# Optimization experiments

Hardware: AMD Instinct MI355X
Metric: run time of the kernel (lower is better)

## Reference

```python
import jax, jax.numpy as jnp
import numpy as np

SEQ, B, I, H = 2048, 64, 512, 512


def setup_inputs() -> dict:
    key = jax.random.key(0)
    ks = jax.random.split(key, 5)
    s = 1.0 / np.sqrt(H)  # torch.nn.RNN init scale
    return {
        "x": jax.random.normal(ks[0], (SEQ, B, I), dtype=jnp.float32),
        "W_ih": jax.random.normal(ks[1], (H, I), dtype=jnp.float32) * s,
        "W_hh": jax.random.normal(ks[2], (H, H), dtype=jnp.float32) * s,
        "b_ih": jax.random.normal(ks[3], (H,), dtype=jnp.float32) * s,
        "b_hh": jax.random.normal(ks[4], (H,), dtype=jnp.float32) * s,
    }


def reference(x, W_ih, W_hh, b_ih, b_hh):
    # Precompute input projection for all timesteps in one big GEMM: [T,B,H]
    xw = jnp.einsum("tbi,hi->tbh", x, W_ih) + b_ih + b_hh

    def step(h, xt):
        # h: [B,H]; xt: [B,H] (already includes x_t W_ih^T + biases)
        h = jnp.tanh(xt + h @ W_hh.T)
        return h, h

    h0 = jnp.zeros((x.shape[1], W_hh.shape[0]), dtype=x.dtype)
    _, out = jax.lax.scan(step, h0, xw)  # out: [T,B,H]
    return out.reshape(-1, W_hh.shape[0])  # [T*B, H], matches out.view(-1, hidden)
```

## Files before the change

kernel.cpp:

```cpp
#include <hip/hip_runtime.h>
#include <cmath>


#define SEQ_T 2048
#define BATCH 64
#define KDIM 512
#define HDIM 512

typedef __fp16 h2v __attribute__((ext_vector_type(2)));
typedef __fp16 f16x8 __attribute__((ext_vector_type(8)));
typedef float f32x4 __attribute__((ext_vector_type(4)));

static __device__ __forceinline__ f16x8 pk8(float4 a, float4 b) {
  h2v p0 = __builtin_amdgcn_cvt_pkrtz(a.x, a.y);
  h2v p1 = __builtin_amdgcn_cvt_pkrtz(a.z, a.w);
  h2v p2 = __builtin_amdgcn_cvt_pkrtz(b.x, b.y);
  h2v p3 = __builtin_amdgcn_cvt_pkrtz(b.z, b.w);
  f16x8 r;
  r[0] = p0[0]; r[1] = p0[1]; r[2] = p1[0]; r[3] = p1[1];
  r[4] = p2[0]; r[5] = p2[1]; r[6] = p3[0]; r[7] = p3[1];
  return r;
}

__global__ __launch_bounds__(256) void w_prep(const float* __restrict__ Whh,
                                              f16x8* __restrict__ ws) {
  int v = blockIdx.x * 256 + threadIdx.x;
  int l = v & 63, w = (v >> 6) & 7, c = (v >> 9) & 3, n = (v >> 11) + 8;
  int row = 64 * w + 16 * c + (l & 15);
  int col = 32 * n + 8 * (l >> 4);
  const float* p = Whh + (size_t)row * KDIM + col;
  ws[v] = pk8(*(const float4*)p, *(const float4*)(p + 4));
}

#define G_LDA 72

#define MFM(mt, nt) \
  d##mt##nt = __builtin_amdgcn_mfma_f32_16x16x32_f16(fa##mt, fb##nt, d##mt##nt, 0, 0, 0);

#define EPI(mt, nt, bb)                                                     \
  {                                                                         \
    int row = m0 + wm + mt * 16 + (l >> 4) * 4;                             \
    int col = n0 + wn + nt * 16 + (l & 15);                                 \
    out[(size_t)(row + 0) * HDIM + col] = d##mt##nt[0] + bb;                \
    out[(size_t)(row + 1) * HDIM + col] = d##mt##nt[1] + bb;                \
    out[(size_t)(row + 2) * HDIM + col] = d##mt##nt[2] + bb;                \
    out[(size_t)(row + 3) * HDIM + col] = d##mt##nt[3] + bb;                \
  }

__global__ __launch_bounds__(256) void xw_gemm(const float* __restrict__ x,
                                               const float* __restrict__ Wih,
                                               const float* __restrict__ bih,
                                               const float* __restrict__ bhh,
                                               float* __restrict__ out) {
  __shared__ __fp16 At[128 * G_LDA];
  __shared__ __fp16 Bt[64 * G_LDA];
  const int tid = threadIdx.x;
  const int l = tid & 63;
  const int w = tid >> 6;
  const int m0 = (blockIdx.x >> 3) * 128;
  const int n0 = (blockIdx.x & 7) * 64;
  const int wm = (w >> 1) * 64;
  const int wn = (w & 1) * 32;

  const float bias0 = bih[n0 + wn + (l & 15)] + bhh[n0 + wn + (l & 15)];
  const float bias1 = bih[n0 + wn + 16 + (l & 15)] + bhh[n0 + wn + 16 + (l & 15)];

  f32x4 d00 = {0,0,0,0}, d01 = {0,0,0,0}, d10 = {0,0,0,0}, d11 = {0,0,0,0};
  f32x4 d20 = {0,0,0,0}, d21 = {0,0,0,0}, d30 = {0,0,0,0}, d31 = {0,0,0,0};

  for (int k0 = 0; k0 < KDIM; k0 += 64) {
    __syncthreads();
#pragma unroll
    for (int p = 0; p < 4; ++p) {
      int idx = tid + p * 256;
      int r = idx >> 3, sg = idx & 7;
      const float* ps = x + (size_t)(m0 + r) * KDIM + k0 + sg * 8;
      *(f16x8*)(At + r * G_LDA + sg * 8) =
          pk8(*(const float4*)ps, *(const float4*)(ps + 4));
    }
#pragma unroll
    for (int p = 0; p < 2; ++p) {
      int idx = tid + p * 256;
      int r = idx >> 3, sg = idx & 7;
      const float* ps = Wih + (size_t)(n0 + r) * KDIM + k0 + sg * 8;
      *(f16x8*)(Bt + r * G_LDA + sg * 8) =
          pk8(*(const float4*)ps, *(const float4*)(ps + 4));
    }
    __syncthreads();
#pragma unroll
    for (int kk = 0; kk < 2; ++kk) {
      const int kc = kk * 32 + (l >> 4) * 8;
      f16x8 fa0 = *(const f16x8*)(At + (wm + 0 * 16 + (l & 15)) * G_LDA + kc);
      f16x8 fa1 = *(const f16x8*)(At + (wm + 1 * 16 + (l & 15)) * G_LDA + kc);
      f16x8 fa2 = *(const f16x8*)(At + (wm + 2 * 16 + (l & 15)) * G_LDA + kc);
      f16x8 fa3 = *(const f16x8*)(At + (wm + 3 * 16 + (l & 15)) * G_LDA + kc);
      f16x8 fb0 = *(const f16x8*)(Bt + (wn + 0 * 16 + (l & 15)) * G_LDA + kc);
      f16x8 fb1 = *(const f16x8*)(Bt + (wn + 1 * 16 + (l & 15)) * G_LDA + kc);
      MFM(0, 0) MFM(1, 0) MFM(2, 0) MFM(3, 0)
      MFM(0, 1) MFM(1, 1) MFM(2, 1) MFM(3, 1)
    }
  }

  EPI(0, 0, bias0) EPI(1, 0, bias0) EPI(2, 0, bias0) EPI(3, 0, bias0)
  EPI(0, 1, bias1) EPI(1, 1, bias1) EPI(2, 1, bias1) EPI(3, 1, bias1)
}


#define REPB(M, c) M(c,0) M(c,1) M(c,2) M(c,3) M(c,4) M(c,5) M(c,6) M(c,7)
#define REPW(M, c) M(c,8) M(c,9) M(c,10) M(c,11)

#define DECLB(c, n) f16x8 bf##c##_##n;
#define LOADB(c, n)                                        \
  {                                                        \
    const float* p = wr##c + 32 * n;                       \
    bf##c##_##n = pk8(*(const float4*)p, *(const float4*)(p + 4)); \
  }
#define LOADW(c, n) bf##c##_##n = wsp[(((n) - 8) * 4 + (c)) * 512];
#define STOREB(c, n)                                                        \
  {                                                                         \
    const float* p = wr##c + 32 * n;                                        \
    *(f16x8*)(ldsm + (((n) - 12) * 4 + c) * 8192 + (tid << 4)) =            \
        pk8(*(const float4*)p, *(const float4*)(p + 4));                    \
  }

#define MF(c, n) \
  d##c = __builtin_amdgcn_mfma_f32_16x16x32_f16(acur, bf##c##_##n, d##c, 0, 0, 0);
#define MFL(c, n)                                                              \
  {                                                                            \
    f16x8 bl = *(const f16x8*)(ldsm + (((n) - 12) * 4 + c) * 8192 + (tid << 4)); \
    d##c = __builtin_amdgcn_mfma_f32_16x16x32_f16(acur, bl, d##c, 0, 0, 0);    \
  }

#define CH(n, nn)                                                \
  {                                                              \
    f16x8 anx = *(const f16x8*)(hcv + 64 * (nn) + goff);         \
    MF(0, n) MF(1, n) MF(2, n) MF(3, n)                          \
    acur = anx;                                                  \
  }
#define CHL(n, nn)                                               \
  {                                                              \
    f16x8 anx = *(const f16x8*)(hcv + 64 * (nn) + goff);         \
    MFL(0, n) MFL(1, n) MFL(2, n) MFL(3, n)                      \
    acur = anx;                                                  \
  }

#define WLDS_BYTES (16 * 8192)
#define HBUF0 WLDS_BYTES
#define LDS_TOTAL (WLDS_BYTES + 3 * 1024)

__global__ __attribute__((amdgpu_flat_work_group_size(512, 512),
                          amdgpu_waves_per_eu(2, 2)))
void rnn_scan(const float* __restrict__ Whh, const f16x8* __restrict__ ws,
              float* __restrict__ io) {
  extern __shared__ __align__(16) char ldsm[];
  const int tid = threadIdx.x;
  const int b = blockIdx.x;
  const int l = tid & 63;
  const int w = tid >> 6;
  const int m16 = l & 15;
  const int gh = l >> 4;
  const int goff = gh << 4;
  const int rb = w << 6;
  const int jo = rb + l;

  const float* wr0 = Whh + (size_t)(rb + 0 + m16) * KDIM + 8 * gh;
  const float* wr1 = Whh + (size_t)(rb + 16 + m16) * KDIM + 8 * gh;
  const float* wr2 = Whh + (size_t)(rb + 32 + m16) * KDIM + 8 * gh;
  const float* wr3 = Whh + (size_t)(rb + 48 + m16) * KDIM + 8 * gh;
  const f16x8* wsp = ws + (w * 64 + l);

  REPB(DECLB, 0) REPB(DECLB, 1) REPB(DECLB, 2) REPB(DECLB, 3)
  REPW(DECLB, 0) REPW(DECLB, 1) REPW(DECLB, 2) REPW(DECLB, 3)
  REPB(LOADB, 0) REPB(LOADB, 1) REPB(LOADB, 2) REPB(LOADB, 3)
  REPW(LOADW, 0) REPW(LOADW, 1) REPW(LOADW, 2) REPW(LOADW, 3)

  STOREB(0, 12) STOREB(1, 12) STOREB(2, 12) STOREB(3, 12)
  STOREB(0, 13) STOREB(1, 13) STOREB(2, 13) STOREB(3, 13)
  STOREB(0, 14) STOREB(1, 14) STOREB(2, 14) STOREB(3, 14)
  STOREB(0, 15) STOREB(1, 15) STOREB(2, 15) STOREB(3, 15)

  if (tid < 512) ((unsigned short*)(ldsm + HBUF0))[tid] = 0;
  __syncthreads();

  char* hcur = ldsm + HBUF0;
  char* hnxt = ldsm + HBUF0 + 1024;
  char* hthr = ldsm + HBUF0 + 2048;

  float* iorow = io + (size_t)b * HDIM;

  for (int t = 0; t < SEQ_T; ++t) {
    float uin = iorow[jo];

    const char* hcv = hcur;
    f16x8 acur = *(const f16x8*)(hcv + goff);

    f32x4 d0 = {0.f, 0.f, 0.f, 0.f};
    f32x4 d1 = {0.f, 0.f, 0.f, 0.f};
    f32x4 d2 = {0.f, 0.f, 0.f, 0.f};
    f32x4 d3 = {0.f, 0.f, 0.f, 0.f};

    CH(0, 1)  CH(1, 2)   CH(2, 3)   CH(3, 4)
    CH(4, 5)  CH(5, 6)   CH(6, 7)   CH(7, 8)
    CH(8, 9)  CH(9, 10)  CH(10, 11) CH(11, 12)
    CHL(12, 13) CHL(13, 14) CHL(14, 15) CHL(15, 15)

    float za = (l & 16) ? d1[0] : d0[0];
    float zb = (l & 16) ? d3[0] : d2[0];
    float zs = (l & 32) ? zb : za;

    float z = uin + zs;
    float e = __expf(2.0f * z);
    float hn = 1.0f - 2.0f * __builtin_amdgcn_rcpf(e + 1.0f);
    iorow[jo] = hn;
    *(__fp16*)(hnxt + 2 * jo) = (__fp16)hn;

    char* tmp = hcur;
    hcur = hnxt; hnxt = hthr; hthr = tmp;
    iorow += (size_t)BATCH * HDIM;
    __syncthreads();
  }
}

extern "C" void kernel_launch(void* const* d_in, const int* in_sizes, int n_in,
                              void* d_out, int out_size, void* d_ws, size_t ws_size,
                              hipStream_t stream) {
  const float* x = (const float*)d_in[0];
  const float* Wih = (const float*)d_in[1];
  const float* Whh = (const float*)d_in[2];
  const float* bih = (const float*)d_in[3];
  const float* bhh = (const float*)d_in[4];
  float* out = (float*)d_out;
  f16x8* ws = (f16x8*)d_ws;

  (void)hipFuncSetAttribute((const void*)rnn_scan,
                            hipFuncAttributeMaxDynamicSharedMemorySize,
                            LDS_TOTAL);

  w_prep<<<32, 256, 0, stream>>>(Whh, ws);

  const int M = SEQ_T * BATCH;
  dim3 g1((M / 128) * (HDIM / 64));
  xw_gemm<<<g1, 256, 0, stream>>>(x, Wih, bih, bhh, out);

  rnn_scan<<<BATCH, 512, LDS_TOTAL, stream>>>(Whh, ws, out);
}
```

Baseline: 3.361 ms.

## Stream W_hh chunks 8-11 from global each step and use lighter barrier

Chunks 8-11 of the recurrent weights are no longer held in registers for the whole kernel. They are now reloaded from the fp16 workspace every timestep, right after they are consumed, so the global loads overlap the remaining MFMAs. The chunk order is changed so these chunks run first. The intent is to free register pressure, or at least reload them cheaply through L2. The __syncthreads is replaced with a manual lgkmcnt wait plus s_barrier fenced by sched_barriers. This adds global memory traffic on every step of a serial, latency-bound loop.

```diff
diff --git a/kernel.cpp b/kernel.cpp
--- a/kernel.cpp
+++ b/kernel.cpp
@@ -107,7 +107,6 @@
 
 
 #define REPB(M, c) M(c,0) M(c,1) M(c,2) M(c,3) M(c,4) M(c,5) M(c,6) M(c,7)
-#define REPW(M, c) M(c,8) M(c,9) M(c,10) M(c,11)
 
 #define DECLB(c, n) f16x8 bf##c##_##n;
 #define LOADB(c, n)                                        \
@@ -115,7 +114,6 @@
     const float* p = wr##c + 32 * n;                       \
     bf##c##_##n = pk8(*(const float4*)p, *(const float4*)(p + 4)); \
   }
-#define LOADW(c, n) bf##c##_##n = wsp[(((n) - 8) * 4 + (c)) * 512];
 #define STOREB(c, n)                                                        \
   {                                                                         \
     const float* p = wr##c + 32 * n;                                        \
@@ -123,8 +121,17 @@
         pk8(*(const float4*)p, *(const float4*)(p + 4));                    \
   }
 
+#define DECLS(n) f16x8 sv0_##n, sv1_##n, sv2_##n, sv3_##n;
+#define LOADS(n)                                   \
+  sv0_##n = wsp[((n - 8) * 4 + 0) * 512];          \
+  sv1_##n = wsp[((n - 8) * 4 + 1) * 512];          \
+  sv2_##n = wsp[((n - 8) * 4 + 2) * 512];          \
+  sv3_##n = wsp[((n - 8) * 4 + 3) * 512];
+
 #define MF(c, n) \
   d##c = __builtin_amdgcn_mfma_f32_16x16x32_f16(acur, bf##c##_##n, d##c, 0, 0, 0);
+#define MSV(c, n) \
+  d##c = __builtin_amdgcn_mfma_f32_16x16x32_f16(acur, sv##c##_##n, d##c, 0, 0, 0);
 #define MFL(c, n)                                                              \
   {                                                                            \
     f16x8 bl = *(const f16x8*)(ldsm + (((n) - 12) * 4 + c) * 8192 + (tid << 4)); \
@@ -137,6 +144,12 @@
     MF(0, n) MF(1, n) MF(2, n) MF(3, n)                          \
     acur = anx;                                                  \
   }
+#define CSV(n, nn)                                               \
+  {                                                              \
+    f16x8 anx = *(const f16x8*)(hcv + 64 * (nn) + goff);         \
+    MSV(0, n) MSV(1, n) MSV(2, n) MSV(3, n)                      \
+    acur = anx;                                                  \
+  }
 #define CHL(n, nn)                                               \
   {                                                              \
     f16x8 anx = *(const f16x8*)(hcv + 64 * (nn) + goff);         \
@@ -147,6 +160,12 @@
 #define WLDS_BYTES (16 * 8192)
 #define HBUF0 WLDS_BYTES
 #define LDS_TOTAL (WLDS_BYTES + 3 * 1024)
+
+#define BAR()                                              \
+  asm volatile("s_waitcnt lgkmcnt(0)" ::: "memory");       \
+  __builtin_amdgcn_sched_barrier(0);                       \
+  __builtin_amdgcn_s_barrier();                            \
+  __builtin_amdgcn_sched_barrier(0);
 
 __global__ __attribute__((amdgpu_flat_work_group_size(512, 512),
                           amdgpu_waves_per_eu(2, 2)))
@@ -170,9 +189,10 @@
   const f16x8* wsp = ws + (w * 64 + l);
 
   REPB(DECLB, 0) REPB(DECLB, 1) REPB(DECLB, 2) REPB(DECLB, 3)
-  REPW(DECLB, 0) REPW(DECLB, 1) REPW(DECLB, 2) REPW(DECLB, 3)
   REPB(LOADB, 0) REPB(LOADB, 1) REPB(LOADB, 2) REPB(LOADB, 3)
-  REPW(LOADW, 0) REPW(LOADW, 1) REPW(LOADW, 2) REPW(LOADW, 3)
+
+  DECLS(8) DECLS(9) DECLS(10) DECLS(11)
+  LOADS(8) LOADS(9) LOADS(10) LOADS(11)
 
   STOREB(0, 12) STOREB(1, 12) STOREB(2, 12) STOREB(3, 12)
   STOREB(0, 13) STOREB(1, 13) STOREB(2, 13) STOREB(3, 13)
@@ -192,16 +212,17 @@
     float uin = iorow[jo];
 
     const char* hcv = hcur;
-    f16x8 acur = *(const f16x8*)(hcv + goff);
+    f16x8 acur = *(const f16x8*)(hcv + 64 * 8 + goff);
 
     f32x4 d0 = {0.f, 0.f, 0.f, 0.f};
     f32x4 d1 = {0.f, 0.f, 0.f, 0.f};
     f32x4 d2 = {0.f, 0.f, 0.f, 0.f};
     f32x4 d3 = {0.f, 0.f, 0.f, 0.f};
 
-    CH(0, 1)  CH(1, 2)   CH(2, 3)   CH(3, 4)
-    CH(4, 5)  CH(5, 6)   CH(6, 7)   CH(7, 8)
-    CH(8, 9)  CH(9, 10)  CH(10, 11) CH(11, 12)
+    CSV(8, 9) CSV(9, 10) CSV(10, 11) CSV(11, 0)
+    LOADS(8) LOADS(9) LOADS(10) LOADS(11)
+    CH(0, 1)  CH(1, 2)  CH(2, 3)  CH(3, 4)
+    CH(4, 5)  CH(5, 6)  CH(6, 7)  CH(7, 12)
     CHL(12, 13) CHL(13, 14) CHL(14, 15) CHL(15, 15)
 
     float za = (l & 16) ? d1[0] : d0[0];
@@ -217,7 +238,7 @@
     char* tmp = hcur;
     hcur = hnxt; hnxt = hthr; hthr = tmp;
     iorow += (size_t)BATCH * HDIM;
-    __syncthreads();
+    BAR();
   }
 }
 
```

New measurement: 3.524 ms. +4.8%, slower.
